# Kernel optimization log

Hardware: AMD Instinct MI355X
Metric: run time of the kernel (lower is better)

The kernel has to match this reference:

```python
import jax, jax.numpy as jnp
import numpy as np

EMBED_DIM = 128
NUM_HEADS = 16
D_K = EMBED_DIM // NUM_HEADS  # 8 qubits per head
DEPTH = 2

# Sign matrix for PauliZ expectations: wire w corresponds to bit (D_K-1-w) of the
# flattened state index (wire 0 = most significant axis, torchquantum convention).
_idx = np.arange(2 ** D_K)
_SIGNS = np.stack([1.0 - 2.0 * ((_idx >> (D_K - 1 - w)) & 1) for w in range(D_K)], axis=1).astype(np.float32)  # [2^d_k, d_k]


def quantum_layer(tokens, qparams):
    """Simulate the variational circuit for a batch of tokens.
    tokens: [N, d_k] real angles; qparams: [depth, d_k] trainable RX angles.
    RX(a)RX(b)=RX(a+b) on the same wire, so encoder + all depth RX layers
    compose into a single RX per wire. Then `depth` CNOT ladders, then <Z_w>.
    """
    theta = tokens + jnp.sum(qparams, axis=0)  # [N, d_k]
    half = 0.5 * theta
    # single-qubit amplitudes after RX(theta)|0>: [cos(t/2), -i sin(t/2)]
    amp = jnp.stack([jnp.cos(half).astype(jnp.complex64),
                     (-1j) * jnp.sin(half).astype(jnp.complex64)], axis=-1)  # [N, d_k, 2]
    # build product state [N, 2, 2, ..., 2]
    state = amp[:, 0, :]
    for i in range(1, D_K):
        state = jnp.einsum('n...,nq->n...q', state, amp[:, i, :])
    # depth x CNOT ladder: CNOT(i, i+1) for i in 0..d_k-2
    for _ in range(DEPTH):
        for i in range(D_K - 1):
            c_ax = 1 + i
            c0 = jnp.take(state, 0, axis=c_ax)
            c1 = jnp.take(state, 1, axis=c_ax)
            c1 = jnp.flip(c1, axis=c_ax)  # target axis = c_ax+1, shifted by -1 after take
            state = jnp.stack([c0, c1], axis=c_ax)
    probs = (state.real ** 2 + state.imag ** 2).reshape(state.shape[0], -1)  # [N, 2^d_k]
    return probs @ jnp.asarray(_SIGNS)  # [N, d_k]


def setup_inputs() -> dict:
    key = jax.random.key(0)
    ks = jax.random.split(key, 6)
    B, S, E = 4, 512, EMBED_DIM
    scale = 1.0 / np.sqrt(E)
    return {
        'x': jax.random.normal(ks[0], (B, S, E), dtype=jnp.float32),
        'Wq': jax.random.normal(ks[1], (E, E), dtype=jnp.float32) * scale,
        'Wk': jax.random.normal(ks[2], (E, E), dtype=jnp.float32) * scale,
        'Wv': jax.random.normal(ks[3], (E, E), dtype=jnp.float32) * scale,
        'Wo': jax.random.normal(ks[4], (E, E), dtype=jnp.float32) * scale,
        'qparams': jax.random.normal(ks[5], (DEPTH, D_K), dtype=jnp.float32),
    }


def reference(x, Wq, Wk, Wv, Wo, qparams):
    B, S, E = x.shape
    H, dk = NUM_HEADS, D_K
    # linear projections (torch Linear, no bias): y = x @ W.T
    q = (x @ Wq.T).reshape(B, S, H, dk).transpose(0, 2, 1, 3)  # [B,H,S,dk]
    k = (x @ Wk.T).reshape(B, S, H, dk).transpose(0, 2, 1, 3)
    v = (x @ Wv.T).reshape(B, S, H, dk).transpose(0, 2, 1, 3)
    # batched quantum circuit over all (batch, head, seq) tokens; shared weights
    qq = quantum_layer(q.reshape(-1, dk), qparams).reshape(B, H, S, dk)
    kq = quantum_layer(k.reshape(-1, dk), qparams).reshape(B, H, S, dk)
    vq = quantum_layer(v.reshape(-1, dk), qparams).reshape(B, H, S, dk)
    scores = jnp.einsum('bhqd,bhkd->bhqk', qq, kq) / jnp.sqrt(jnp.float32(dk))
    attn = jax.nn.softmax(scores, axis=-1)  # dropout in eval mode: identity
    out = jnp.einsum('bhqk,bhkd->bhqd', attn, vq)
    out = out.transpose(0, 2, 1, 3).reshape(B, S, E)
    return out @ Wo.T
```

## Files before the change

### kernel.cpp

```cpp
#include <hip/hip_runtime.h>
#include <cmath>

#define MATSZ 262144
#define QKV_OFF 65536
#define AOUT_OFF (65536 + 3 * MATSZ)

__global__ __launch_bounds__(256, 3) void k_qkvq(
    const float* __restrict__ x, const float* __restrict__ Wq,
    const float* __restrict__ Wk, const float* __restrict__ Wv,
    const float* __restrict__ qp, float* __restrict__ ws) {
  __shared__ float xs[8][128];
  __shared__ float th[2][8][128];
  const int t = threadIdx.x;
  const int tile = blockIdx.x;
  const int m = blockIdx.y;
  const float* W = (m == 0) ? Wq : (m == 1) ? Wk : Wv;
  {
    ((float4*)&xs[0][0])[t] = ((const float4*)(x + (size_t)tile * 1024))[t];
  }
  const int e = t & 127, half = t >> 7;
  float4 w[16];
  {
    const float4* wr = (const float4*)W + (size_t)e * 32 + half * 16;
#pragma unroll
    for (int i = 0; i < 16; ++i) w[i] = wr[i];
  }
  __syncthreads();
  const float4* xs4 = (const float4*)&xs[0][0];
#pragma unroll
  for (int r = 0; r < 8; ++r) {
    float a = 0.f;
    const float4* xr = xs4 + r * 32 + half * 16;
#pragma unroll
    for (int i = 0; i < 16; ++i) {
      float4 xv = xr[i];
      a = fmaf(xv.x, w[i].x, a);
      a = fmaf(xv.y, w[i].y, a);
      a = fmaf(xv.z, w[i].z, a);
      a = fmaf(xv.w, w[i].w, a);
    }
    th[half][r][e] = a;
  }
  __syncthreads();
  const int cg = t & 31, rg = t >> 5;
  const float4* th4 = (const float4*)&th[0][0][0];
  float4 s0 = th4[rg * 32 + cg];
  float4 s1 = th4[256 + rg * 32 + cg];
  float4 a4 = make_float4(s0.x + s1.x, s0.y + s1.y, s0.z + s1.z, s0.w + s1.w);
  const int j0 = (cg & 1) * 4;
  float4 qs;
  qs.x = qp[j0 + 0] + qp[8 + j0 + 0];
  qs.y = qp[j0 + 1] + qp[8 + j0 + 1];
  qs.z = qp[j0 + 2] + qp[8 + j0 + 2];
  qs.w = qp[j0 + 3] + qp[8 + j0 + 3];
  float4 c;
  c.x = __cosf(a4.x + qs.x);
  c.y = __cosf(a4.y + qs.y);
  c.z = __cosf(a4.z + qs.z);
  c.w = __cosf(a4.w + qs.w);
  float4 u;
  u.x = c.x; u.y = c.y; u.z = c.x * c.z; u.w = c.y * c.w;
  float gz = __shfl_xor(u.z, 1);
  float gw = __shfl_xor(u.w, 1);
  const bool hi = (cg & 1) != 0;
  float mz = hi ? gz : 1.f, mw = hi ? gw : 1.f;
  float4 o;
  o.x = u.x * mz; o.y = u.y * mw; o.z = u.z * mz; o.w = u.w * mw;
  const int h = cg >> 1;
  int row = tile * 8 + rg;
  int b = row >> 9, s = row & 511;
  float* dst = ws + QKV_OFF + (size_t)m * MATSZ +
               ((size_t)((b << 4) + h) * 512 + s) * 8 + (hi ? 4 : 0);
  *(float4*)dst = o;
}

__global__ __launch_bounds__(256, 4) void k_attn(
    float* __restrict__ ws) {
  __shared__ float4 kslo[512], kshi[512], vslo[512], vshi[512];
  const int qt = blockIdx.x;
  const int bh = blockIdx.y;
  const float* qkv = ws + QKV_OFF;
  const float* Qg = qkv + (size_t)bh * 4096;
  const float4* Kg = (const float4*)(qkv + MATSZ + (size_t)bh * 4096);
  const float4* Vg = (const float4*)(qkv + 2 * (size_t)MATSZ + (size_t)bh * 4096);
  const int t = threadIdx.x;
  for (int k = t; k < 512; k += 256) {
    kslo[k] = Kg[2 * k]; kshi[k] = Kg[2 * k + 1];
    vslo[k] = Vg[2 * k]; vshi[k] = Vg[2 * k + 1];
  }
  __syncthreads();
  const int qslot = t >> 4, ko = t & 15;
  const int row0 = qt * 64 + qslot * 4;
  const float scale = 0.35355339059327373f;
  float4 qa[4], qb[4];
#pragma unroll
  for (int r = 0; r < 4; ++r) {
    qa[r] = ((const float4*)(Qg + (size_t)(row0 + r) * 8))[0];
    qb[r] = ((const float4*)(Qg + (size_t)(row0 + r) * 8))[1];
    qa[r].x *= scale; qa[r].y *= scale; qa[r].z *= scale; qa[r].w *= scale;
    qb[r].x *= scale; qb[r].y *= scale; qb[r].z *= scale; qb[r].w *= scale;
  }
  float l[4] = {0.f, 0.f, 0.f, 0.f};
  float a[4][8];
#pragma unroll
  for (int r = 0; r < 4; ++r)
#pragma unroll
    for (int j = 0; j < 8; ++j) a[r][j] = 0.f;
#pragma unroll 2
  for (int i = 0; i < 32; ++i) {
    int k = i * 16 + ko;
    float4 kx = kslo[k], ky = kshi[k];
    float4 vx = vslo[k], vy = vshi[k];
#pragma unroll
    for (int r = 0; r < 4; ++r) {
      float s = qa[r].x * kx.x + qa[r].y * kx.y + qa[r].z * kx.z + qa[r].w * kx.w +
                qb[r].x * ky.x + qb[r].y * ky.y + qb[r].z * ky.z + qb[r].w * ky.w;
      float p = __expf(s);
      l[r] += p;
      a[r][0] = fmaf(p, vx.x, a[r][0]);
      a[r][1] = fmaf(p, vx.y, a[r][1]);
      a[r][2] = fmaf(p, vx.z, a[r][2]);
      a[r][3] = fmaf(p, vx.w, a[r][3]);
      a[r][4] = fmaf(p, vy.x, a[r][4]);
      a[r][5] = fmaf(p, vy.y, a[r][5]);
      a[r][6] = fmaf(p, vy.z, a[r][6]);
      a[r][7] = fmaf(p, vy.w, a[r][7]);
    }
  }
#pragma unroll
  for (int mm = 1; mm <= 8; mm <<= 1) {
#pragma unroll
    for (int r = 0; r < 4; ++r) {
      l[r] += __shfl_xor(l[r], mm);
#pragma unroll
      for (int j = 0; j < 8; ++j) a[r][j] += __shfl_xor(a[r][j], mm);
    }
  }
  if (ko == 0) {
    int b = bh >> 4, h = bh & 15;
    float* aout = ws + AOUT_OFF;
#pragma unroll
    for (int r = 0; r < 4; ++r) {
      float inv = 1.f / l[r];
      float* d = aout + ((size_t)(b * 512 + row0 + r)) * 128 + h * 8;
      ((float4*)d)[0] = make_float4(a[r][0] * inv, a[r][1] * inv,
                                    a[r][2] * inv, a[r][3] * inv);
      ((float4*)d)[1] = make_float4(a[r][4] * inv, a[r][5] * inv,
                                    a[r][6] * inv, a[r][7] * inv);
    }
  }
}

__global__ __launch_bounds__(256, 3) void k_out(
    const float* __restrict__ ws, const float* __restrict__ Wo,
    float* __restrict__ out) {
  __shared__ float as_[8][128];
  __shared__ float th[2][8][128];
  const int t = threadIdx.x;
  const int tile = blockIdx.x;
  const float* aout = ws + AOUT_OFF;
  {
    ((float4*)&as_[0][0])[t] = ((const float4*)(aout + (size_t)tile * 1024))[t];
  }
  const int e = t & 127, half = t >> 7;
  float4 w[16];
  {
    const float4* wr = (const float4*)Wo + (size_t)e * 32 + half * 16;
#pragma unroll
    for (int i = 0; i < 16; ++i) w[i] = wr[i];
  }
  __syncthreads();
  const float4* as4 = (const float4*)&as_[0][0];
#pragma unroll
  for (int r = 0; r < 8; ++r) {
    float a = 0.f;
    const float4* ar = as4 + r * 32 + half * 16;
#pragma unroll
    for (int i = 0; i < 16; ++i) {
      float4 av = ar[i];
      a = fmaf(av.x, w[i].x, a);
      a = fmaf(av.y, w[i].y, a);
      a = fmaf(av.z, w[i].z, a);
      a = fmaf(av.w, w[i].w, a);
    }
    th[half][r][e] = a;
  }
  __syncthreads();
  const int cg = t & 31, rg = t >> 5;
  const float4* th4 = (const float4*)&th[0][0][0];
  float4 s0 = th4[rg * 32 + cg];
  float4 s1 = th4[256 + rg * 32 + cg];
  float4 o = make_float4(s0.x + s1.x, s0.y + s1.y, s0.z + s1.z, s0.w + s1.w);
  ((float4*)(out + (size_t)(tile * 8 + rg) * 128))[cg] = o;
}

extern "C" void kernel_launch(void* const* d_in, const int* in_sizes, int n_in,
                              void* d_out, int out_size, void* d_ws, size_t ws_size,
                              hipStream_t stream) {
  const float* x  = (const float*)d_in[0];
  const float* Wq = (const float*)d_in[1];
  const float* Wk = (const float*)d_in[2];
  const float* Wv = (const float*)d_in[3];
  const float* Wo = (const float*)d_in[4];
  const float* qp = (const float*)d_in[5];
  float* out = (float*)d_out;
  float* ws = (float*)d_ws;

  hipLaunchKernelGGL(k_qkvq, dim3(256, 3), dim3(256), 0, stream,
                     x, Wq, Wk, Wv, qp, ws);
  hipLaunchKernelGGL(k_attn, dim3(8, 64), dim3(256), 0, stream, ws);
  hipLaunchKernelGGL(k_out, dim3(256), dim3(256), 0, stream, ws, Wo, out);
}
```

Baseline: 41.61 us.

## Fuse output projection into attention kernel via atomic completion counters

Result: slower. 75.35 us (+81.1%).

```diff
diff --git a/kernel.cpp b/kernel.cpp
--- a/kernel.cpp
+++ b/kernel.cpp
@@ -2,8 +2,9 @@
 #include <cmath>
 
 #define MATSZ 262144
-#define QKV_OFF 65536
-#define AOUT_OFF (65536 + 3 * MATSZ)
+#define QKV_OFF 0
+#define AOUT_OFF (3 * MATSZ)
+#define CNT_OFF (4 * MATSZ)
 
 __global__ __launch_bounds__(256, 3) void k_qkvq(
     const float* __restrict__ x, const float* __restrict__ Wq,
@@ -14,6 +15,9 @@
   const int t = threadIdx.x;
   const int tile = blockIdx.x;
   const int m = blockIdx.y;
+  if (blockIdx.x == 0 && blockIdx.y == 0) {
+    ((int*)(ws + CNT_OFF))[t] = 0;
+  }
   const float* W = (m == 0) ? Wq : (m == 1) ? Wk : Wv;
   {
     ((float4*)&xs[0][0])[t] = ((const float4*)(x + (size_t)tile * 1024))[t];
@@ -74,16 +78,24 @@
   *(float4*)dst = o;
 }
 
-__global__ __launch_bounds__(256, 4) void k_attn(
-    float* __restrict__ ws) {
-  __shared__ float4 kslo[512], kshi[512], vslo[512], vshi[512];
+__global__ __launch_bounds__(256, 4) void k_attn_out(
+    float* __restrict__ ws, const float* __restrict__ Wo,
+    float* __restrict__ out) {
+  __shared__ float4 smv[2048];
+  __shared__ int finmask;
+  float4* kslo = smv;
+  float4* kshi = smv + 512;
+  float4* vslo = smv + 1024;
+  float4* vshi = smv + 1536;
   const int qt = blockIdx.x;
   const int bh = blockIdx.y;
+  const int b = bh >> 4;
   const float* qkv = ws + QKV_OFF;
   const float* Qg = qkv + (size_t)bh * 4096;
   const float4* Kg = (const float4*)(qkv + MATSZ + (size_t)bh * 4096);
   const float4* Vg = (const float4*)(qkv + 2 * (size_t)MATSZ + (size_t)bh * 4096);
   const int t = threadIdx.x;
+  if (t == 0) finmask = 0;
   for (int k = t; k < 512; k += 256) {
     kslo[k] = Kg[2 * k]; kshi[k] = Kg[2 * k + 1];
     vslo[k] = Vg[2 * k]; vshi[k] = Vg[2 * k + 1];
@@ -137,61 +149,71 @@
     }
   }
   if (ko == 0) {
-    int b = bh >> 4, h = bh & 15;
-    float* aout = ws + AOUT_OFF;
+    float* aout2 = ws + AOUT_OFF + (size_t)bh * 4096;
 #pragma unroll
     for (int r = 0; r < 4; ++r) {
       float inv = 1.f / l[r];
-      float* d = aout + ((size_t)(b * 512 + row0 + r)) * 128 + h * 8;
+      float* d = aout2 + (size_t)(row0 + r) * 8;
       ((float4*)d)[0] = make_float4(a[r][0] * inv, a[r][1] * inv,
                                     a[r][2] * inv, a[r][3] * inv);
       ((float4*)d)[1] = make_float4(a[r][4] * inv, a[r][5] * inv,
                                     a[r][6] * inv, a[r][7] * inv);
     }
   }
-}
-
-__global__ __launch_bounds__(256, 3) void k_out(
-    const float* __restrict__ ws, const float* __restrict__ Wo,
-    float* __restrict__ out) {
-  __shared__ float as_[8][128];
-  __shared__ float th[2][8][128];
-  const int t = threadIdx.x;
-  const int tile = blockIdx.x;
-  const float* aout = ws + AOUT_OFF;
-  {
-    ((float4*)&as_[0][0])[t] = ((const float4*)(aout + (size_t)tile * 1024))[t];
-  }
-  const int e = t & 127, half = t >> 7;
-  float4 w[16];
-  {
+  __syncthreads();
+  int* cnt = (int*)(ws + CNT_OFF);
+  if (t < 8) {
+    __threadfence();
+    int old = atomicAdd(&cnt[b * 64 + qt * 8 + t], 1);
+    if (old == 15) atomicOr(&finmask, 1 << t);
+  }
+  __syncthreads();
+  int fm = finmask;
+  if (fm == 0) return;
+  __threadfence();
+  float* at = (float*)smv;
+  float* th = (float*)smv + 1024;
+  const float* aoutb = ws + AOUT_OFF;
+  while (fm) {
+    int i = __ffs(fm) - 1;
+    fm &= fm - 1;
+    const int s0 = qt * 64 + i * 8;
+    __syncthreads();
+    if (t < 128) {
+      int h = t >> 3, r = t & 7;
+      const float4* src =
+          (const float4*)(aoutb + ((size_t)(b * 16 + h) * 512 + s0 + r) * 8);
+      float4* dst = (float4*)(at + r * 128 + h * 8);
+      dst[0] = src[0];
+      dst[1] = src[1];
+    }
+    __syncthreads();
+    const int e = t & 127, half = t >> 7;
     const float4* wr = (const float4*)Wo + (size_t)e * 32 + half * 16;
-#pragma unroll
-    for (int i = 0; i < 16; ++i) w[i] = wr[i];
-  }
-  __syncthreads();
-  const float4* as4 = (const float4*)&as_[0][0];
-#pragma unroll
-  for (int r = 0; r < 8; ++r) {
-    float a = 0.f;
-    const float4* ar = as4 + r * 32 + half * 16;
-#pragma unroll
-    for (int i = 0; i < 16; ++i) {
-      float4 av = ar[i];
-      a = fmaf(av.x, w[i].x, a);
-      a = fmaf(av.y, w[i].y, a);
-      a = fmaf(av.z, w[i].z, a);
-      a = fmaf(av.w, w[i].w, a);
-    }
-    th[half][r][e] = a;
-  }
-  __syncthreads();
-  const int cg = t & 31, rg = t >> 5;
-  const float4* th4 = (const float4*)&th[0][0][0];
-  float4 s0 = th4[rg * 32 + cg];
-  float4 s1 = th4[256 + rg * 32 + cg];
-  float4 o = make_float4(s0.x + s1.x, s0.y + s1.y, s0.z + s1.z, s0.w + s1.w);
-  ((float4*)(out + (size_t)(tile * 8 + rg) * 128))[cg] = o;
+    const float4* at4 = (const float4*)at;
+#pragma unroll
+    for (int r = 0; r < 8; ++r) {
+      float acc = 0.f;
+      const float4* ar = at4 + r * 32 + half * 16;
+#pragma unroll
+      for (int ii = 0; ii < 16; ++ii) {
+        float4 av = ar[ii];
+        float4 wv = wr[ii];
+        acc = fmaf(av.x, wv.x, acc);
+        acc = fmaf(av.y, wv.y, acc);
+        acc = fmaf(av.z, wv.z, acc);
+        acc = fmaf(av.w, wv.w, acc);
+      }
+      th[(half * 8 + r) * 128 + e] = acc;
+    }
+    __syncthreads();
+    const int cg = t & 31, rg = t >> 5;
+    const float4* th4 = (const float4*)th;
+    float4 p0 = th4[rg * 32 + cg];
+    float4 p1 = th4[256 + rg * 32 + cg];
+    float4 o = make_float4(p0.x + p1.x, p0.y + p1.y, p0.z + p1.z, p0.w + p1.w);
+    ((float4*)(out + (size_t)(b * 512 + s0 + rg) * 128))[cg] = o;
+  }
 }
 
 extern "C" void kernel_launch(void* const* d_in, const int* in_sizes, int n_in,
@@ -208,6 +230,6 @@
 
   hipLaunchKernelGGL(k_qkvq, dim3(256, 3), dim3(256), 0, stream,
                      x, Wq, Wk, Wv, qp, ws);
-  hipLaunchKernelGGL(k_attn, dim3(8, 64), dim3(256), 0, stream, ws);
-  hipLaunchKernelGGL(k_out, dim3(256), dim3(256), 0, stream, ws, Wo, out);
+  hipLaunchKernelGGL(k_attn_out, dim3(8, 64), dim3(256), 0, stream,
+                     ws, Wo, out);
 }
```

## Fuse attention with output projection and double-buffer K/V tiles

Applied to the files above, without the earlier changes.

Measured after the change: 73.14 us. +75.8%, slower.

```diff
diff --git a/kernel.cpp b/kernel.cpp
--- a/kernel.cpp
+++ b/kernel.cpp
@@ -2,22 +2,20 @@
 #include <cmath>
 
 #define MATSZ 262144
-#define QKV_OFF 65536
-#define AOUT_OFF (65536 + 3 * MATSZ)
+
+#define CH  8448
+#define LDK 132
 
 __global__ __launch_bounds__(256, 3) void k_qkvq(
     const float* __restrict__ x, const float* __restrict__ Wq,
     const float* __restrict__ Wk, const float* __restrict__ Wv,
     const float* __restrict__ qp, float* __restrict__ ws) {
-  __shared__ float xs[8][128];
-  __shared__ float th[2][8][128];
+  __shared__ float xs[16][128];
+  __shared__ float th[2][16][128];
   const int t = threadIdx.x;
   const int tile = blockIdx.x;
   const int m = blockIdx.y;
   const float* W = (m == 0) ? Wq : (m == 1) ? Wk : Wv;
-  {
-    ((float4*)&xs[0][0])[t] = ((const float4*)(x + (size_t)tile * 1024))[t];
-  }
   const int e = t & 127, half = t >> 7;
   float4 w[16];
   {
@@ -25,10 +23,16 @@
 #pragma unroll
     for (int i = 0; i < 16; ++i) w[i] = wr[i];
   }
+  {
+    const float4* xg = (const float4*)(x + (size_t)tile * 2048);
+    float4* xv = (float4*)&xs[0][0];
+    xv[t] = xg[t];
+    xv[t + 256] = xg[t + 256];
+  }
   __syncthreads();
   const float4* xs4 = (const float4*)&xs[0][0];
 #pragma unroll
-  for (int r = 0; r < 8; ++r) {
+  for (int r = 0; r < 16; ++r) {
     float a = 0.f;
     const float4* xr = xs4 + r * 32 + half * 16;
 #pragma unroll
@@ -42,156 +46,184 @@
     th[half][r][e] = a;
   }
   __syncthreads();
-  const int cg = t & 31, rg = t >> 5;
+  const int cg = t & 31;
+  const int r0 = (t >> 5) * 2;
+  const int j0 = (cg & 1) * 4;
+  float4 qs4;
+  qs4.x = qp[j0 + 0] + qp[8 + j0 + 0];
+  qs4.y = qp[j0 + 1] + qp[8 + j0 + 1];
+  qs4.z = qp[j0 + 2] + qp[8 + j0 + 2];
+  qs4.w = qp[j0 + 3] + qp[8 + j0 + 3];
+  const bool hi = (cg & 1) != 0;
+  const float osc = (m == 0) ? 0.51013389376f : 1.0f;
   const float4* th4 = (const float4*)&th[0][0][0];
-  float4 s0 = th4[rg * 32 + cg];
-  float4 s1 = th4[256 + rg * 32 + cg];
-  float4 a4 = make_float4(s0.x + s1.x, s0.y + s1.y, s0.z + s1.z, s0.w + s1.w);
-  const int j0 = (cg & 1) * 4;
-  float4 qs;
-  qs.x = qp[j0 + 0] + qp[8 + j0 + 0];
-  qs.y = qp[j0 + 1] + qp[8 + j0 + 1];
-  qs.z = qp[j0 + 2] + qp[8 + j0 + 2];
-  qs.w = qp[j0 + 3] + qp[8 + j0 + 3];
-  float4 c;
-  c.x = __cosf(a4.x + qs.x);
-  c.y = __cosf(a4.y + qs.y);
-  c.z = __cosf(a4.z + qs.z);
-  c.w = __cosf(a4.w + qs.w);
-  float4 u;
-  u.x = c.x; u.y = c.y; u.z = c.x * c.z; u.w = c.y * c.w;
-  float gz = __shfl_xor(u.z, 1);
-  float gw = __shfl_xor(u.w, 1);
-  const bool hi = (cg & 1) != 0;
-  float mz = hi ? gz : 1.f, mw = hi ? gw : 1.f;
-  float4 o;
-  o.x = u.x * mz; o.y = u.y * mw; o.z = u.z * mz; o.w = u.w * mw;
-  const int h = cg >> 1;
-  int row = tile * 8 + rg;
-  int b = row >> 9, s = row & 511;
-  float* dst = ws + QKV_OFF + (size_t)m * MATSZ +
-               ((size_t)((b << 4) + h) * 512 + s) * 8 + (hi ? 4 : 0);
-  *(float4*)dst = o;
+#pragma unroll
+  for (int rr = 0; rr < 2; ++rr) {
+    int r = r0 + rr;
+    float4 s0 = th4[r * 32 + cg];
+    float4 s1 = th4[512 + r * 32 + cg];
+    float4 a4 = make_float4(s0.x + s1.x, s0.y + s1.y, s0.z + s1.z, s0.w + s1.w);
+    float4 c;
+    c.x = __cosf(a4.x + qs4.x);
+    c.y = __cosf(a4.y + qs4.y);
+    c.z = __cosf(a4.z + qs4.z);
+    c.w = __cosf(a4.w + qs4.w);
+    float4 u;
+    u.x = c.x; u.y = c.y; u.z = c.x * c.z; u.w = c.y * c.w;
+    float gz = __shfl_xor(u.z, 1);
+    float gw = __shfl_xor(u.w, 1);
+    float mz = hi ? gz : 1.f, mw = hi ? gw : 1.f;
+    float4 o;
+    o.x = u.x * mz * osc; o.y = u.y * mw * osc;
+    o.z = u.z * mz * osc; o.w = u.w * mw * osc;
+    int row = tile * 16 + r;
+    *(float4*)(ws + (size_t)m * MATSZ + (size_t)row * 128 + cg * 4) = o;
+  }
 }
 
-__global__ __launch_bounds__(256, 4) void k_attn(
-    float* __restrict__ ws) {
-  __shared__ float4 kslo[512], kshi[512], vslo[512], vshi[512];
-  const int qt = blockIdx.x;
-  const int bh = blockIdx.y;
-  const float* qkv = ws + QKV_OFF;
-  const float* Qg = qkv + (size_t)bh * 4096;
-  const float4* Kg = (const float4*)(qkv + MATSZ + (size_t)bh * 4096);
-  const float4* Vg = (const float4*)(qkv + 2 * (size_t)MATSZ + (size_t)bh * 4096);
+__global__ __launch_bounds__(256, 1) void k_fused(
+    const float* __restrict__ ws, const float* __restrict__ Wo,
+    float* __restrict__ out) {
+  extern __shared__ float sm[];
   const int t = threadIdx.x;
-  for (int k = t; k < 512; k += 256) {
-    kslo[k] = Kg[2 * k]; kshi[k] = Kg[2 * k + 1];
-    vslo[k] = Vg[2 * k]; vshi[k] = Vg[2 * k + 1];
-  }
-  __syncthreads();
-  const int qslot = t >> 4, ko = t & 15;
-  const int row0 = qt * 64 + qslot * 4;
-  const float scale = 0.35355339059327373f;
-  float4 qa[4], qb[4];
-#pragma unroll
-  for (int r = 0; r < 4; ++r) {
-    qa[r] = ((const float4*)(Qg + (size_t)(row0 + r) * 8))[0];
-    qb[r] = ((const float4*)(Qg + (size_t)(row0 + r) * 8))[1];
-    qa[r].x *= scale; qa[r].y *= scale; qa[r].z *= scale; qa[r].w *= scale;
-    qb[r].x *= scale; qb[r].y *= scale; qb[r].z *= scale; qb[r].w *= scale;
-  }
-  float l[4] = {0.f, 0.f, 0.f, 0.f};
-  float a[4][8];
-#pragma unroll
-  for (int r = 0; r < 4; ++r)
+  const int b = blockIdx.x >> 6;
+  const int row0 = (blockIdx.x & 63) * 8;
+  const float* Qg = ws + ((size_t)(b * 512 + row0)) * 128;
+  const float* Kg = ws + MATSZ + (size_t)b * 512 * 128;
+  const float* Vg = ws + 2 * (size_t)MATSZ + (size_t)b * 512 * 128;
+  float* qs = sm + 4 * CH;
+  ((float4*)qs)[t] = ((const float4*)Qg)[t];
+  {
+    const float4* Ks = (const float4*)Kg;
+    const float4* Vs = (const float4*)Vg;
+#pragma unroll
+    for (int i = 0; i < 8; ++i) {
+      int idx = t + i * 256;
+      int r = idx >> 5, c4 = idx & 31;
+      *(float4*)(sm + (size_t)r * LDK + c4 * 4) = Ks[idx];
+      *(float4*)(sm + CH + (size_t)r * LDK + c4 * 4) = Vs[idx];
+    }
+  }
+  __syncthreads();
+  const int h = t >> 4, ko = t & 15;
+  float4 qa[8], qb[8];
+#pragma unroll
+  for (int r = 0; r < 8; ++r) {
+    qa[r] = *(const float4*)(qs + r * 128 + h * 8);
+    qb[r] = *(const float4*)(qs + r * 128 + h * 8 + 4);
+  }
+  float l[8];
+  float a[8][8];
+#pragma unroll
+  for (int r = 0; r < 8; ++r) {
+    l[r] = 0.f;
 #pragma unroll
     for (int j = 0; j < 8; ++j) a[r][j] = 0.f;
-#pragma unroll 2
-  for (int i = 0; i < 32; ++i) {
-    int k = i * 16 + ko;
-    float4 kx = kslo[k], ky = kshi[k];
-    float4 vx = vslo[k], vy = vshi[k];
-#pragma unroll
-    for (int r = 0; r < 4; ++r) {
-      float s = qa[r].x * kx.x + qa[r].y * kx.y + qa[r].z * kx.z + qa[r].w * kx.w +
-                qb[r].x * ky.x + qb[r].y * ky.y + qb[r].z * ky.z + qb[r].w * ky.w;
-      float p = __expf(s);
-      l[r] += p;
-      a[r][0] = fmaf(p, vx.x, a[r][0]);
-      a[r][1] = fmaf(p, vx.y, a[r][1]);
-      a[r][2] = fmaf(p, vx.z, a[r][2]);
-      a[r][3] = fmaf(p, vx.w, a[r][3]);
-      a[r][4] = fmaf(p, vy.x, a[r][4]);
-      a[r][5] = fmaf(p, vy.y, a[r][5]);
-      a[r][6] = fmaf(p, vy.z, a[r][6]);
-      a[r][7] = fmaf(p, vy.w, a[r][7]);
-    }
+  }
+  for (int c = 0; c < 8; ++c) {
+    const float* KB = sm + (size_t)(c & 1) * (2 * CH);
+    const float* VB = KB + CH;
+    const bool more = (c < 7);
+    float4 tk[8], tv[8];
+    if (more) {
+      const float4* Ks = (const float4*)Kg + (size_t)(c + 1) * 2048;
+      const float4* Vs = (const float4*)Vg + (size_t)(c + 1) * 2048;
+#pragma unroll
+      for (int i = 0; i < 8; ++i) {
+        int idx = t + i * 256;
+        tk[i] = Ks[idx];
+        tv[i] = Vs[idx];
+      }
+    }
+#pragma unroll
+    for (int i = 0; i < 4; ++i) {
+      int j = i * 16 + ko;
+      float4 kx = *(const float4*)(KB + j * LDK + h * 8);
+      float4 ky = *(const float4*)(KB + j * LDK + h * 8 + 4);
+      float4 vx = *(const float4*)(VB + j * LDK + h * 8);
+      float4 vy = *(const float4*)(VB + j * LDK + h * 8 + 4);
+#pragma unroll
+      for (int r = 0; r < 8; ++r) {
+        float s = qa[r].x * kx.x + qa[r].y * kx.y + qa[r].z * kx.z +
+                  qa[r].w * kx.w + qb[r].x * ky.x + qb[r].y * ky.y +
+                  qb[r].z * ky.z + qb[r].w * ky.w;
+        float p = exp2f(s);
+        l[r] += p;
+        a[r][0] = fmaf(p, vx.x, a[r][0]);
+        a[r][1] = fmaf(p, vx.y, a[r][1]);
+        a[r][2] = fmaf(p, vx.z, a[r][2]);
+        a[r][3] = fmaf(p, vx.w, a[r][3]);
+        a[r][4] = fmaf(p, vy.x, a[r][4]);
+        a[r][5] = fmaf(p, vy.y, a[r][5]);
+        a[r][6] = fmaf(p, vy.z, a[r][6]);
+        a[r][7] = fmaf(p, vy.w, a[r][7]);
+      }
+    }
+    if (more) {
+      float* KN = sm + (size_t)((c + 1) & 1) * (2 * CH);
+#pragma unroll
+      for (int i = 0; i < 8; ++i) {
+        int idx = t + i * 256;
+        int r = idx >> 5, c4 = idx & 31;
+        *(float4*)(KN + (size_t)r * LDK + c4 * 4) = tk[i];
+        *(float4*)(KN + CH + (size_t)r * LDK + c4 * 4) = tv[i];
+      }
+    }
+    __syncthreads();
+  }
+  const int e = t & 127, half = t >> 7;
+  float4 w[16];
+  {
+    const float4* wr = (const float4*)Wo + (size_t)e * 32 + half * 16;
+#pragma unroll
+    for (int i = 0; i < 16; ++i) w[i] = wr[i];
   }
 #pragma unroll
   for (int mm = 1; mm <= 8; mm <<= 1) {
 #pragma unroll
-    for (int r = 0; r < 4; ++r) {
+    for (int r = 0; r < 8; ++r) {
       l[r] += __shfl_xor(l[r], mm);
 #pragma unroll
       for (int j = 0; j < 8; ++j) a[r][j] += __shfl_xor(a[r][j], mm);
     }
   }
   if (ko == 0) {
-    int b = bh >> 4, h = bh & 15;
-    float* aout = ws + AOUT_OFF;
-#pragma unroll
-    for (int r = 0; r < 4; ++r) {
+#pragma unroll
+    for (int r = 0; r < 8; ++r) {
       float inv = 1.f / l[r];
-      float* d = aout + ((size_t)(b * 512 + row0 + r)) * 128 + h * 8;
+      float* d = sm + r * 128 + h * 8;
       ((float4*)d)[0] = make_float4(a[r][0] * inv, a[r][1] * inv,
                                     a[r][2] * inv, a[r][3] * inv);
       ((float4*)d)[1] = make_float4(a[r][4] * inv, a[r][5] * inv,
                                     a[r][6] * inv, a[r][7] * inv);
     }
   }
-}
-
-__global__ __launch_bounds__(256, 3) void k_out(
-    const float* __restrict__ ws, const float* __restrict__ Wo,
-    float* __restrict__ out) {
-  __shared__ float as_[8][128];
-  __shared__ float th[2][8][128];
-  const int t = threadIdx.x;
-  const int tile = blockIdx.x;
-  const float* aout = ws + AOUT_OFF;
-  {
-    ((float4*)&as_[0][0])[t] = ((const float4*)(aout + (size_t)tile * 1024))[t];
-  }
-  const int e = t & 127, half = t >> 7;
-  float4 w[16];
-  {
-    const float4* wr = (const float4*)Wo + (size_t)e * 32 + half * 16;
-#pragma unroll
-    for (int i = 0; i < 16; ++i) w[i] = wr[i];
-  }
-  __syncthreads();
-  const float4* as4 = (const float4*)&as_[0][0];
+  __syncthreads();
+  float* th = sm + 1024;
+  const float4* at4 = (const float4*)sm;
 #pragma unroll
   for (int r = 0; r < 8; ++r) {
-    float a = 0.f;
-    const float4* ar = as4 + r * 32 + half * 16;
+    float acc = 0.f;
+    const float4* ar = at4 + r * 32 + half * 16;
 #pragma unroll
     for (int i = 0; i < 16; ++i) {
       float4 av = ar[i];
-      a = fmaf(av.x, w[i].x, a);
-      a = fmaf(av.y, w[i].y, a);
-      a = fmaf(av.z, w[i].z, a);
-      a = fmaf(av.w, w[i].w, a);
-    }
-    th[half][r][e] = a;
-  }
-  __syncthreads();
-  const int cg = t & 31, rg = t >> 5;
-  const float4* th4 = (const float4*)&th[0][0][0];
-  float4 s0 = th4[rg * 32 + cg];
-  float4 s1 = th4[256 + rg * 32 + cg];
-  float4 o = make_float4(s0.x + s1.x, s0.y + s1.y, s0.z + s1.z, s0.w + s1.w);
-  ((float4*)(out + (size_t)(tile * 8 + rg) * 128))[cg] = o;
+      acc = fmaf(av.x, w[i].x, acc);
+      acc = fmaf(av.y, w[i].y, acc);
+      acc = fmaf(av.z, w[i].z, acc);
+      acc = fmaf(av.w, w[i].w, acc);
+    }
+    th[(half * 8 + r) * 128 + e] = acc;
+  }
+  __syncthreads();
+  {
+    const int cg = t & 31, rg = t >> 5;
+    const float4* th4 = (const float4*)th;
+    float4 p0 = th4[rg * 32 + cg];
+    float4 p1 = th4[256 + rg * 32 + cg];
+    float4 o = make_float4(p0.x + p1.x, p0.y + p1.y, p0.z + p1.z, p0.w + p1.w);
+    *(float4*)(out + ((size_t)(b * 512 + row0 + rg)) * 128 + cg * 4) = o;
+  }
 }
 
 extern "C" void kernel_launch(void* const* d_in, const int* in_sizes, int n_in,
@@ -206,8 +238,15 @@
   float* out = (float*)d_out;
   float* ws = (float*)d_ws;
 
-  hipLaunchKernelGGL(k_qkvq, dim3(256, 3), dim3(256), 0, stream,
+  const size_t smem = (4 * CH + 1024) * sizeof(float);
+  static int attr_done = 0;
+  (void)hipFuncSetAttribute((const void*)k_fused,
+                            hipFuncAttributeMaxDynamicSharedMemorySize,
+                            (int)smem);
+  (void)attr_done;
+
+  hipLaunchKernelGGL(k_qkvq, dim3(128, 3), dim3(256), 0, stream,
                      x, Wq, Wk, Wv, qp, ws);
-  hipLaunchKernelGGL(k_attn, dim3(8, 64), dim3(256), 0, stream, ws);
-  hipLaunchKernelGGL(k_out, dim3(256), dim3(256), 0, stream, ws, Wo, out);
+  hipLaunchKernelGGL(k_fused, dim3(256), dim3(256), smem, stream,
+                     ws, Wo, out);
 }
```
